# Performance work log

Hardware: AMD Instinct MI355X
Metric: run time of the kernel (lower is better)

Reference implementation:

```python
import jax, jax.numpy as jnp
import numpy as np

LAMBDA = 0.5
TAU = 1.0
EPS = 1e-8  # torch F.cosine_similarity eps

B, D = 8192, 1024


def setup_inputs() -> dict:
    key = jax.random.key(0)
    k1, k2, k3, k4 = jax.random.split(key, 4)
    return {
        "student_query_emb": jax.random.normal(k1, (B, D), dtype=jnp.float32),
        "student_passage_emb": jax.random.normal(k2, (B, D), dtype=jnp.float32),
        "teacher_query_emb": jax.random.normal(k3, (B, D), dtype=jnp.float32),
        "teacher_passage_emb": jax.random.normal(k4, (B, D), dtype=jnp.float32),
    }


def _mse(a, b):
    d = a - b
    return jnp.mean(d * d)


def _retrieval_loss(q, p):
    # cosine sim = (q . p) / max(||q|| * ||p||, eps); normalize then matmul
    # (avoids the [B,B,D] broadcast intermediate of the torch version)
    qn = q / jnp.maximum(jnp.linalg.norm(q, axis=-1, keepdims=True), EPS)
    pn = p / jnp.maximum(jnp.linalg.norm(p, axis=-1, keepdims=True), EPS)
    logits = jnp.einsum("bd,cd->bc", qn, pn) / TAU  # [B, B]
    # cross-entropy with labels = arange(B): pick the diagonal log-prob
    logprobs = jax.nn.log_softmax(logits, axis=-1)
    return -jnp.mean(jnp.diagonal(logprobs))


def reference(student_query_emb, student_passage_emb, teacher_query_emb, teacher_passage_emb):
    distill = 0.5 * (_mse(student_query_emb, teacher_query_emb)
                     + _mse(student_passage_emb, teacher_passage_emb))
    retrieval = _retrieval_loss(student_query_emb, student_passage_emb)
    return LAMBDA * distill + (1.0 - LAMBDA) * retrieval
```

## Files before the change

### kernel.cpp

```cpp
#include <hip/hip_runtime.h>
#include <hip/hip_bf16.h>

typedef unsigned short u16;
typedef unsigned char u8;
typedef float f32x4 __attribute__((ext_vector_type(4)));
typedef int int4v __attribute__((ext_vector_type(4)));
typedef int int8v __attribute__((ext_vector_type(8)));

#define B_ROWS 8192
#define D_DIM  1024
#define FP8_SCALE 16.0f
#define ACC_UNSCALE (1.0f/256.0f)


__global__ void __launch_bounds__(256) prep_kernel(
    const float* __restrict__ sq, const float* __restrict__ sp,
    const float* __restrict__ tq, const float* __restrict__ tp,
    int* __restrict__ qn, int* __restrict__ pn,
    float* __restrict__ ppq, float* __restrict__ ppp, float* __restrict__ ppd)
{
    const int wave = threadIdx.x >> 6;
    const int l    = threadIdx.x & 63;
    const int r    = blockIdx.x * 4 + wave;
    const size_t rb4 = (size_t)r * (D_DIM / 4);

    const float4* Q4 = (const float4*)sq + rb4;
    const float4* P4 = (const float4*)sp + rb4;
    const float4* A4 = (const float4*)tq + rb4;
    const float4* B4 = (const float4*)tp + rb4;

    float4 qv[4], pv[4];
    float sq2 = 0.f, sp2 = 0.f, dq = 0.f, dp = 0.f, qp = 0.f;
    #pragma unroll
    for (int j = 0; j < 4; ++j) {
        const int idx = j * 64 + l;
        float4 q = Q4[idx], p = P4[idx], a = A4[idx], b = B4[idx];
        qv[j] = q; pv[j] = p;
        sq2 += q.x*q.x + q.y*q.y + q.z*q.z + q.w*q.w;
        sp2 += p.x*p.x + p.y*p.y + p.z*p.z + p.w*p.w;
        float dx = q.x-a.x, dy = q.y-a.y, dz = q.z-a.z, dw = q.w-a.w;
        dq += dx*dx + dy*dy + dz*dz + dw*dw;
        dx = p.x-b.x; dy = p.y-b.y; dz = p.z-b.z; dw = p.w-b.w;
        dp += dx*dx + dy*dy + dz*dz + dw*dw;
        qp += q.x*p.x + q.y*p.y + q.z*p.z + q.w*p.w;
    }

    #pragma unroll
    for (int m = 1; m <= 32; m <<= 1) {
        sq2 += __shfl_xor(sq2, m);
        sp2 += __shfl_xor(sp2, m);
        dq  += __shfl_xor(dq, m);
        dp  += __shfl_xor(dp, m);
        qp  += __shfl_xor(qp, m);
    }

    const float rq = 1.0f / fmaxf(sqrtf(sq2), 1e-8f);
    const float rp = 1.0f / fmaxf(sqrtf(sp2), 1e-8f);

    if (l == 0) {
        ppq[r] = dq;
        ppp[r] = dp;
        ppd[r] = qp * rq * rp;
    }

    const float fq = rq * FP8_SCALE;
    const float fp = rp * FP8_SCALE;
    int* qrow = qn + (size_t)r * (D_DIM / 4);
    int* prow = pn + (size_t)r * (D_DIM / 4);
    #pragma unroll
    for (int j = 0; j < 4; ++j) {
        const int idx = j * 64 + l;
        int pk = __builtin_amdgcn_cvt_pk_fp8_f32(qv[j].x * fq, qv[j].y * fq, 0, false);
        pk     = __builtin_amdgcn_cvt_pk_fp8_f32(qv[j].z * fq, qv[j].w * fq, pk, true);
        qrow[idx] = pk;
        pk = __builtin_amdgcn_cvt_pk_fp8_f32(pv[j].x * fp, pv[j].y * fp, 0, false);
        pk = __builtin_amdgcn_cvt_pk_fp8_f32(pv[j].z * fp, pv[j].w * fp, pk, true);
        prow[idx] = pk;
    }
}

union Frag { int8v v8; struct { int4v lo, hi; } h; };

__global__ void __launch_bounds__(512, 2) gemm_rowsum_kernel(
    const u8* __restrict__ Q, const u8* __restrict__ P,
    float* __restrict__ gpart)
{
    __shared__ u8 smA[2][256 * 128];

    const int tid  = threadIdx.x;
    const int wave = tid >> 6;
    const int lane = tid & 63;
    const int wm   = wave >> 2;
    const int wn   = wave & 3;

    const int bid = blockIdx.x;
    const int xcd = bid & 7;
    const int idx = bid >> 3;
    const int bn  = (xcd << 2) | (idx & 3);
    const int bm  = idx >> 2;

    const int srow   = tid >> 3;
    const int schunk = (tid & 7) ^ (srow & 7);
    const u8* Ag = Q + (size_t)(bm * 256 + srow) * D_DIM + schunk * 16;
    const int ldsw = wave * 1024;

#define STAGE_A(b, rbase, k0)                                                  \
    __builtin_amdgcn_global_load_lds(                                          \
        (const __attribute__((address_space(1))) void*)(Ag + (size_t)(rbase) * D_DIM + (k0)), \
        (__attribute__((address_space(3))) void*)(&smA[b][(rbase) * 128] + ldsw), 16, 0, 0)

    const int quad = lane >> 4;
    const int rw   = lane & 15;
    const int r7   = lane & 7;
    const int off_lo = ((2 * quad) ^ r7) * 16;
    const int off_hi = ((2 * quad + 1) ^ r7) * 16;
    const int arow_base = (wm * 128 + rw) * 128;

    const u8* Bd = P + (size_t)(bn * 256 + wn * 64 + rw) * D_DIM + quad * 32;

    f32x4 acc[8][4];
    #pragma unroll
    for (int i = 0; i < 8; ++i)
        #pragma unroll
        for (int j = 0; j < 4; ++j)
            acc[i][j] = (f32x4){0.f, 0.f, 0.f, 0.f};

    STAGE_A(0, 0, 0);   STAGE_A(0, 64, 0);   STAGE_A(0, 128, 0);   STAGE_A(0, 192, 0);
    STAGE_A(1, 0, 128); STAGE_A(1, 64, 128); STAGE_A(1, 128, 128); STAGE_A(1, 192, 128);

#define SB0 __builtin_amdgcn_sched_barrier(0);

#define MFMA_HALF(mih)                                                         \
    __builtin_amdgcn_s_setprio(1);                                             \
    _Pragma("unroll")                                                          \
    for (int mi = 0; mi < 4; ++mi)                                             \
      _Pragma("unroll")                                                        \
      for (int ni = 0; ni < 4; ++ni)                                           \
        acc[(mih)*4 + mi][ni] =                                                \
            __builtin_amdgcn_mfma_scale_f32_16x16x128_f8f6f4(                  \
                af[(mih)*4 + mi].v8, b[ni].v8,                                 \
                acc[(mih)*4 + mi][ni],                                         \
                0, 0, 0, 0x7f7f7f7f, 0, 0x7f7f7f7f);                           \
    __builtin_amdgcn_s_setprio(0);

#define KSTEP(t, DO_T2)                                                        \
  {                                                                            \
    constexpr int cur = (t) & 1;                                               \
    const u8* sA_ = &smA[cur][0];                                              \
    Frag af[8], b[4];                                                          \
               \
    _Pragma("unroll")                                                          \
    for (int ni = 0; ni < 4; ++ni) {                                           \
      b[ni].h.lo = *(const int4v*)(Bd + ni * 16 * D_DIM + (t) * 128);          \
      b[ni].h.hi = *(const int4v*)(Bd + ni * 16 * D_DIM + (t) * 128 + 16);     \
    }                                                                          \
            \
    asm volatile("s_waitcnt vmcnt(12)" ::: "memory");                          \
    __builtin_amdgcn_s_barrier();                                              \
    SB0                                                                        \
                  \
    _Pragma("unroll")                                                          \
    for (int mi = 0; mi < 8; ++mi)                                             \
      af[mi].h.lo = *(const int4v*)(sA_ + arow_base + mi * 2048 + off_lo);     \
    SB0                                                                        \
    _Pragma("unroll")                                                          \
    for (int mi = 0; mi < 8; ++mi)                                             \
      af[mi].h.hi = *(const int4v*)(sA_ + arow_base + mi * 2048 + off_hi);     \
    asm volatile("s_waitcnt lgkmcnt(0)" ::: "memory");                         \
    SB0                                                                        \
    __builtin_amdgcn_s_barrier();         \
    MFMA_HALF(0)                                                               \
    if (DO_T2) { STAGE_A(cur, 0,   ((t) + 2) * 128);                           \
                 STAGE_A(cur, 64,  ((t) + 2) * 128);                           \
                 STAGE_A(cur, 128, ((t) + 2) * 128);                           \
                 STAGE_A(cur, 192, ((t) + 2) * 128); }                         \
    MFMA_HALF(1)                                                               \
  }

    KSTEP(0, true)
    KSTEP(1, true)
    KSTEP(2, true)
    KSTEP(3, true)
    KSTEP(4, true)
    KSTEP(5, true)
    KSTEP(6, false)
    KSTEP(7, false)

#undef KSTEP
#undef MFMA_HALF
#undef SB0
#undef STAGE_A

    float esum[8][4];
    #pragma unroll
    for (int mi = 0; mi < 8; ++mi)
        #pragma unroll
        for (int r = 0; r < 4; ++r) {
            float s = 0.f;
            #pragma unroll
            for (int ni = 0; ni < 4; ++ni)
                s += __expf(acc[mi][ni][r] * ACC_UNSCALE);
            esum[mi][r] = s;
        }
    #pragma unroll
    for (int m = 1; m <= 8; m <<= 1)
        #pragma unroll
        for (int mi = 0; mi < 8; ++mi)
            #pragma unroll
            for (int r = 0; r < 4; ++r)
                esum[mi][r] += __shfl_xor(esum[mi][r], m);

    if (rw == 0) {
        float* dst = gpart + (size_t)(bn * 4 + wn) * B_ROWS
                   + bm * 256 + wm * 128;
        #pragma unroll
        for (int mi = 0; mi < 8; ++mi)
            #pragma unroll
            for (int r = 0; r < 4; ++r)
                dst[mi * 16 + quad * 4 + r] = esum[mi][r];
    }
}

__global__ void __launch_bounds__(256) reduce_kernel(
    const float* __restrict__ gpart,
    const float* __restrict__ ppq, const float* __restrict__ ppp,
    const float* __restrict__ ppd, float4* __restrict__ bpart)
{
    const int t = threadIdx.x;
    const int r = blockIdx.x * 256 + t;
    float s = 0.f;
    #pragma unroll 8
    for (int j = 0; j < 128; ++j) s += gpart[(size_t)j * B_ROWS + r];
    float ls = logf(s);
    float v2 = ppq[r], v3 = ppp[r], v4 = ppd[r];
    #pragma unroll
    for (int m = 1; m <= 32; m <<= 1) {
        ls += __shfl_xor(ls, m);
        v2 += __shfl_xor(v2, m);
        v3 += __shfl_xor(v3, m);
        v4 += __shfl_xor(v4, m);
    }
    __shared__ float red[4][4];
    if ((t & 63) == 0) {
        red[t >> 6][0] = ls; red[t >> 6][1] = v2;
        red[t >> 6][2] = v3; red[t >> 6][3] = v4;
    }
    __syncthreads();
    if (t == 0) {
        float4 o;
        o.x = red[0][0] + red[1][0] + red[2][0] + red[3][0];
        o.y = red[0][1] + red[1][1] + red[2][1] + red[3][1];
        o.z = red[0][2] + red[1][2] + red[2][2] + red[3][2];
        o.w = red[0][3] + red[1][3] + red[2][3] + red[3][3];
        bpart[blockIdx.x] = o;
    }
}

__global__ void __launch_bounds__(64) finalize_kernel(
    const float4* __restrict__ bpart, float* __restrict__ out)
{
    const int t = threadIdx.x;
    float4 v = (t < 32) ? bpart[t] : (float4){0.f, 0.f, 0.f, 0.f};
    #pragma unroll
    for (int m = 1; m <= 16; m <<= 1) {
        v.x += __shfl_xor(v.x, m);
        v.y += __shfl_xor(v.y, m);
        v.z += __shfl_xor(v.z, m);
        v.w += __shfl_xor(v.w, m);
    }
    if (t == 0) {
        const float inv_bd = 1.0f / ((float)B_ROWS * (float)D_DIM);
        float distill   = 0.5f * (v.y + v.z) * inv_bd;
        float retrieval = (v.x - v.w) / (float)B_ROWS;
        out[0] = 0.5f * distill + 0.5f * retrieval;
    }
}

extern "C" void kernel_launch(void* const* d_in, const int* in_sizes, int n_in,
                              void* d_out, int out_size, void* d_ws, size_t ws_size,
                              hipStream_t stream) {
    const float* sq = (const float*)d_in[0];
    const float* sp = (const float*)d_in[1];
    const float* tq = (const float*)d_in[2];
    const float* tp = (const float*)d_in[3];

    char* ws = (char*)d_ws;
    float*  ppq   = (float*)(ws);
    float*  ppp   = (float*)(ws + 32768);
    float*  ppd   = (float*)(ws + 65536);
    float4* bpart = (float4*)(ws + 98304);
    float*  gpart = (float*)(ws + 131072);
    int*    qn    = (int*)(ws + 131072 + (size_t)128 * B_ROWS * 4);
    int*    pn    = (int*)((char*)qn + (size_t)B_ROWS * D_DIM);

    prep_kernel<<<B_ROWS / 4, 256, 0, stream>>>(sq, sp, tq, tp, qn, pn, ppq, ppp, ppd);
    gemm_rowsum_kernel<<<1024, 512, 0, stream>>>((const u8*)qn, (const u8*)pn, gpart);
    reduce_kernel<<<32, 256, 0, stream>>>(gpart, ppq, ppp, ppd, bpart);
    finalize_kernel<<<1, 64, 0, stream>>>(bpart, (float*)d_out);
}
```

Measured before the change: 247.6 us.

## Shrink GEMM tile to 128x128 and stage both operands through LDS

```diff
diff --git a/kernel.cpp b/kernel.cpp
--- a/kernel.cpp
+++ b/kernel.cpp
@@ -81,100 +81,97 @@
 
 union Frag { int8v v8; struct { int4v lo, hi; } h; };
 
-__global__ void __launch_bounds__(512, 2) gemm_rowsum_kernel(
+__global__ void __launch_bounds__(256, 3) gemm_rowsum_kernel(
     const u8* __restrict__ Q, const u8* __restrict__ P,
     float* __restrict__ gpart)
 {
-    __shared__ u8 smA[2][256 * 128];
+    __shared__ u8 smA[128 * 128];
+    __shared__ u8 smB[128 * 128];
 
     const int tid  = threadIdx.x;
     const int wave = tid >> 6;
     const int lane = tid & 63;
-    const int wm   = wave >> 2;
-    const int wn   = wave & 3;
-
-    const int bid = blockIdx.x;
-    const int xcd = bid & 7;
-    const int idx = bid >> 3;
-    const int bn  = (xcd << 2) | (idx & 3);
-    const int bm  = idx >> 2;
+    const int wm   = wave >> 1;
+    const int wn   = wave & 1;
+    const int bm   = blockIdx.y;
+    const int bn   = blockIdx.x;
 
     const int srow   = tid >> 3;
     const int schunk = (tid & 7) ^ (srow & 7);
-    const u8* Ag = Q + (size_t)(bm * 256 + srow) * D_DIM + schunk * 16;
+    const u8* Ag = Q + (size_t)(bm * 128 + srow) * D_DIM + schunk * 16;
+    const u8* Bg = P + (size_t)(bn * 128 + srow) * D_DIM + schunk * 16;
     const int ldsw = wave * 1024;
 
-#define STAGE_A(b, rbase, k0)                                                  \
+#define STAGE_A(rbase, k0)                                                     \
     __builtin_amdgcn_global_load_lds(                                          \
         (const __attribute__((address_space(1))) void*)(Ag + (size_t)(rbase) * D_DIM + (k0)), \
-        (__attribute__((address_space(3))) void*)(&smA[b][(rbase) * 128] + ldsw), 16, 0, 0)
+        (__attribute__((address_space(3))) void*)(smA + (rbase) * 128 + ldsw), 16, 0, 0)
+#define STAGE_B(rbase, k0)                                                     \
+    __builtin_amdgcn_global_load_lds(                                          \
+        (const __attribute__((address_space(1))) void*)(Bg + (size_t)(rbase) * D_DIM + (k0)), \
+        (__attribute__((address_space(3))) void*)(smB + (rbase) * 128 + ldsw), 16, 0, 0)
+
+#define STAGE_ALL(k0)                                                          \
+    STAGE_A(0, k0); STAGE_A(32, k0); STAGE_A(64, k0); STAGE_A(96, k0);         \
+    STAGE_B(0, k0); STAGE_B(32, k0); STAGE_B(64, k0); STAGE_B(96, k0);
 
     const int quad = lane >> 4;
     const int rw   = lane & 15;
     const int r7   = lane & 7;
     const int off_lo = ((2 * quad) ^ r7) * 16;
     const int off_hi = ((2 * quad + 1) ^ r7) * 16;
-    const int arow_base = (wm * 128 + rw) * 128;
-
-    const u8* Bd = P + (size_t)(bn * 256 + wn * 64 + rw) * D_DIM + quad * 32;
-
-    f32x4 acc[8][4];
-    #pragma unroll
-    for (int i = 0; i < 8; ++i)
+    const int arow_base = (wm * 64 + rw) * 128;
+    const int brow_base = (wn * 64 + rw) * 128;
+
+    f32x4 acc[4][4];
+    #pragma unroll
+    for (int i = 0; i < 4; ++i)
         #pragma unroll
         for (int j = 0; j < 4; ++j)
             acc[i][j] = (f32x4){0.f, 0.f, 0.f, 0.f};
 
-    STAGE_A(0, 0, 0);   STAGE_A(0, 64, 0);   STAGE_A(0, 128, 0);   STAGE_A(0, 192, 0);
-    STAGE_A(1, 0, 128); STAGE_A(1, 64, 128); STAGE_A(1, 128, 128); STAGE_A(1, 192, 128);
+    STAGE_ALL(0)
 
 #define SB0 __builtin_amdgcn_sched_barrier(0);
 
-#define MFMA_HALF(mih)                                                         \
+#define MFMA1(mi, ni)                                                          \
+    acc[mi][ni] = __builtin_amdgcn_mfma_scale_f32_16x16x128_f8f6f4(            \
+        af[mi].v8, bf[ni].v8, acc[mi][ni],                                     \
+        0, 0, 0, 0x7f7f7f7f, 0, 0x7f7f7f7f);
+
+#define KSTEP(t, DO_NEXT)                                                      \
+  {                                                                            \
+    Frag af[4], bf[4];                                                         \
+                           \
+    asm volatile("s_waitcnt vmcnt(0)" ::: "memory");                           \
+    __builtin_amdgcn_s_barrier();                                              \
+    SB0                                                                        \
+                                    \
+    _Pragma("unroll")                                                          \
+    for (int mi = 0; mi < 4; ++mi)                                             \
+      af[mi].h.lo = *(const int4v*)(smA + arow_base + mi * 2048 + off_lo);     \
+    _Pragma("unroll")                                                          \
+    for (int ni = 0; ni < 4; ++ni)                                             \
+      bf[ni].h.lo = *(const int4v*)(smB + brow_base + ni * 2048 + off_lo);     \
+    SB0                                                                        \
+    _Pragma("unroll")                                                          \
+    for (int mi = 0; mi < 4; ++mi)                                             \
+      af[mi].h.hi = *(const int4v*)(smA + arow_base + mi * 2048 + off_hi);     \
+    _Pragma("unroll")                                                          \
+    for (int ni = 0; ni < 4; ++ni)                                             \
+      bf[ni].h.hi = *(const int4v*)(smB + brow_base + ni * 2048 + off_hi);     \
+    asm volatile("s_waitcnt lgkmcnt(0)" ::: "memory");                         \
+    SB0                                                                        \
+    __builtin_amdgcn_s_barrier();      \
+    SB0                                                                        \
+            \
+    if (DO_NEXT) { STAGE_ALL(((t) + 1) * 128) }                                \
     __builtin_amdgcn_s_setprio(1);                                             \
-    _Pragma("unroll")                                                          \
-    for (int mi = 0; mi < 4; ++mi)                                             \
-      _Pragma("unroll")                                                        \
-      for (int ni = 0; ni < 4; ++ni)                                           \
-        acc[(mih)*4 + mi][ni] =                                                \
-            __builtin_amdgcn_mfma_scale_f32_16x16x128_f8f6f4(                  \
-                af[(mih)*4 + mi].v8, b[ni].v8,                                 \
-                acc[(mih)*4 + mi][ni],                                         \
-                0, 0, 0, 0x7f7f7f7f, 0, 0x7f7f7f7f);                           \
-    __builtin_amdgcn_s_setprio(0);
-
-#define KSTEP(t, DO_T2)                                                        \
-  {                                                                            \
-    constexpr int cur = (t) & 1;                                               \
-    const u8* sA_ = &smA[cur][0];                                              \
-    Frag af[8], b[4];                                                          \
-               \
-    _Pragma("unroll")                                                          \
-    for (int ni = 0; ni < 4; ++ni) {                                           \
-      b[ni].h.lo = *(const int4v*)(Bd + ni * 16 * D_DIM + (t) * 128);          \
-      b[ni].h.hi = *(const int4v*)(Bd + ni * 16 * D_DIM + (t) * 128 + 16);     \
-    }                                                                          \
-            \
-    asm volatile("s_waitcnt vmcnt(12)" ::: "memory");                          \
-    __builtin_amdgcn_s_barrier();                                              \
-    SB0                                                                        \
-                  \
-    _Pragma("unroll")                                                          \
-    for (int mi = 0; mi < 8; ++mi)                                             \
-      af[mi].h.lo = *(const int4v*)(sA_ + arow_base + mi * 2048 + off_lo);     \
-    SB0                                                                        \
-    _Pragma("unroll")                                                          \
-    for (int mi = 0; mi < 8; ++mi)                                             \
-      af[mi].h.hi = *(const int4v*)(sA_ + arow_base + mi * 2048 + off_hi);     \
-    asm volatile("s_waitcnt lgkmcnt(0)" ::: "memory");                         \
-    SB0                                                                        \
-    __builtin_amdgcn_s_barrier();         \
-    MFMA_HALF(0)                                                               \
-    if (DO_T2) { STAGE_A(cur, 0,   ((t) + 2) * 128);                           \
-                 STAGE_A(cur, 64,  ((t) + 2) * 128);                           \
-                 STAGE_A(cur, 128, ((t) + 2) * 128);                           \
-                 STAGE_A(cur, 192, ((t) + 2) * 128); }                         \
-    MFMA_HALF(1)                                                               \
+    MFMA1(0, 0) MFMA1(0, 1) MFMA1(1, 0) MFMA1(1, 1)                            \
+    MFMA1(0, 2) MFMA1(0, 3) MFMA1(1, 2) MFMA1(1, 3)                            \
+    MFMA1(2, 0) MFMA1(2, 1) MFMA1(3, 0) MFMA1(3, 1)                            \
+    MFMA1(2, 2) MFMA1(2, 3) MFMA1(3, 2) MFMA1(3, 3)                            \
+    __builtin_amdgcn_s_setprio(0);                                             \
   }
 
     KSTEP(0, true)
@@ -183,17 +180,19 @@
     KSTEP(3, true)
     KSTEP(4, true)
     KSTEP(5, true)
-    KSTEP(6, false)
+    KSTEP(6, true)
     KSTEP(7, false)
 
 #undef KSTEP
-#undef MFMA_HALF
+#undef MFMA1
 #undef SB0
+#undef STAGE_ALL
 #undef STAGE_A
-
-    float esum[8][4];
-    #pragma unroll
-    for (int mi = 0; mi < 8; ++mi)
+#undef STAGE_B
+
+    float esum[4][4];
+    #pragma unroll
+    for (int mi = 0; mi < 4; ++mi)
         #pragma unroll
         for (int r = 0; r < 4; ++r) {
             float s = 0.f;
@@ -205,16 +204,16 @@
     #pragma unroll
     for (int m = 1; m <= 8; m <<= 1)
         #pragma unroll
-        for (int mi = 0; mi < 8; ++mi)
+        for (int mi = 0; mi < 4; ++mi)
             #pragma unroll
             for (int r = 0; r < 4; ++r)
                 esum[mi][r] += __shfl_xor(esum[mi][r], m);
 
     if (rw == 0) {
-        float* dst = gpart + (size_t)(bn * 4 + wn) * B_ROWS
-                   + bm * 256 + wm * 128;
-        #pragma unroll
-        for (int mi = 0; mi < 8; ++mi)
+        float* dst = gpart + (size_t)(bn * 2 + wn) * B_ROWS
+                   + bm * 128 + wm * 64;
+        #pragma unroll
+        for (int mi = 0; mi < 4; ++mi)
             #pragma unroll
             for (int r = 0; r < 4; ++r)
                 dst[mi * 16 + quad * 4 + r] = esum[mi][r];
@@ -294,7 +293,7 @@
     int*    pn    = (int*)((char*)qn + (size_t)B_ROWS * D_DIM);
 
     prep_kernel<<<B_ROWS / 4, 256, 0, stream>>>(sq, sp, tq, tp, qn, pn, ppq, ppp, ppd);
-    gemm_rowsum_kernel<<<1024, 512, 0, stream>>>((const u8*)qn, (const u8*)pn, gpart);
+    gemm_rowsum_kernel<<<dim3(64, 64), 256, 0, stream>>>((const u8*)qn, (const u8*)pn, gpart);
     reduce_kernel<<<32, 256, 0, stream>>>(gpart, ppq, ppp, ppd, bpart);
     finalize_kernel<<<1, 64, 0, stream>>>(bpart, (float*)d_out);
 }
```

After: 232.0 us (median of 2 runs). 6.3% less time.
